# Optimization experiments

Measured on AMD Instinct MI355X. Metric: run time of the kernel, lower is better.

The kernel has to match this reference:

```python
import jax, jax.numpy as jnp
import numpy as np

SEQ, B, IN_DIM = 100, 2048, 64
MID_I, LATENT, V_MID, V_LAT, MID_O, OUT_DIM = 60, 20, 800, 50, 800, 512


def _lstm_cell(x, h, c, wih, whh, bih, bhh):
    # PyTorch gate order: i, f, g, o
    g = x @ wih.T + h @ whh.T + bih + bhh
    i, f, gg, o = jnp.split(g, 4, axis=-1)
    c = jax.nn.sigmoid(f) * c + jax.nn.sigmoid(i) * jnp.tanh(gg)
    h = jax.nn.sigmoid(o) * jnp.tanh(c)
    return h, c


def _lstm_seq(xs, wih, whh, bih, bhh, hid):
    b = xs.shape[1]
    init = (jnp.zeros((b, hid), xs.dtype), jnp.zeros((b, hid), xs.dtype))
    def step(carry, xt):
        h, c = _lstm_cell(xt, carry[0], carry[1], wih, whh, bih, bhh)
        return (h, c), h
    _, outs = jax.lax.scan(step, init, xs)
    return outs  # (seq, B, hid)


def setup_inputs() -> dict:
    key = jax.random.key(0)
    ks = iter(jax.random.split(key, 40))
    w = lambda shape: jax.random.normal(next(ks), shape, jnp.float32) * 0.05
    p = {}
    p['x'] = jax.random.normal(next(ks), (SEQ, B, IN_DIM), jnp.float32)
    p['fc1_wih'] = w((4 * MID_I, IN_DIM)); p['fc1_whh'] = w((4 * MID_I, MID_I))
    p['fc1_bih'] = w((4 * MID_I,)); p['fc1_bhh'] = w((4 * MID_I,))
    p['fc21_wih'] = w((4 * LATENT, MID_I)); p['fc21_whh'] = w((4 * LATENT, LATENT))
    p['fc21_bih'] = w((4 * LATENT,)); p['fc21_bhh'] = w((4 * LATENT,))
    p['lin1_w'] = w((V_MID, LATENT * SEQ)); p['lin1_b'] = w((V_MID,))
    p['lin2_w'] = w((V_LAT, V_MID)); p['lin2_b'] = w((V_LAT,))
    p['idlin_w'] = w((V_LAT, V_LAT)); p['idlin_b'] = w((V_LAT,))
    p['down1_w'] = w((LATENT, V_LAT)); p['down1_b'] = w((LATENT,))
    p['down2_w'] = w((LATENT, OUT_DIM)); p['down2_b'] = w((LATENT,))
    p['l3_wih'] = w((4 * V_LAT, LATENT)); p['l3_whh'] = w((4 * V_LAT, V_LAT))
    p['l3_bih'] = w((4 * V_LAT,)); p['l3_bhh'] = w((4 * V_LAT,))
    p['l4_wih'] = w((4 * MID_O, V_LAT)); p['l4_whh'] = w((4 * MID_O, MID_O))
    p['l4_bih'] = w((4 * MID_O,)); p['l4_bhh'] = w((4 * MID_O,))
    p['l5_wih'] = w((4 * OUT_DIM, MID_O)); p['l5_whh'] = w((4 * OUT_DIM, OUT_DIM))
    p['l5_bih'] = w((4 * OUT_DIM,)); p['l5_bhh'] = w((4 * OUT_DIM,))
    return p


def reference(x, fc1_wih, fc1_whh, fc1_bih, fc1_bhh,
              fc21_wih, fc21_whh, fc21_bih, fc21_bhh,
              lin1_w, lin1_b, lin2_w, lin2_b,
              idlin_w, idlin_b, down1_w, down1_b, down2_w, down2_b,
              l3_wih, l3_whh, l3_bih, l3_bhh,
              l4_wih, l4_whh, l4_bih, l4_bhh,
              l5_wih, l5_whh, l5_bih, l5_bhh):
    seq, b, _ = x.shape
    # encode
    h1 = jax.nn.relu(_lstm_seq(x, fc1_wih, fc1_whh, fc1_bih, fc1_bhh, MID_I))
    out21 = _lstm_seq(h1, fc21_wih, fc21_whh, fc21_bih, fc21_bhh, LATENT)
    flat = jnp.transpose(out21, (1, 2, 0)).reshape(b, -1)  # (B, latent*seq)
    mu = jax.nn.relu(flat @ lin1_w.T + lin1_b)
    mu = jax.nn.relu(mu @ lin2_w.T + lin2_b)  # (B, v_latent)
    # decode
    h_t = mu
    c_t = mu @ idlin_w.T + idlin_b
    out = mu @ down1_w.T + down1_b
    h2 = jnp.zeros((b, MID_O), mu.dtype); c2 = jnp.zeros((b, MID_O), mu.dtype)
    h3 = jnp.zeros((b, OUT_DIM), mu.dtype); c3 = jnp.zeros((b, OUT_DIM), mu.dtype)
    def step(carry, _):
        h_t, c_t, h2, c2, h3, c3, out = carry
        h_t, c_t = _lstm_cell(out, h_t, c_t, l3_wih, l3_whh, l3_bih, l3_bhh)
        h2, c2 = _lstm_cell(h_t, h2, c2, l4_wih, l4_whh, l4_bih, l4_bhh)
        h3, c3 = _lstm_cell(h2, h3, c3, l5_wih, l5_whh, l5_bih, l5_bhh)
        out = h3 @ down2_w.T + down2_b
        return (h_t, c_t, h2, c2, h3, c3, out), h3
    _, muTheta = jax.lax.scan(step, (h_t, c_t, h2, c2, h3, c3, out), None, length=seq)
    return muTheta, mu
```

## Files before the change

kernel.cpp:

```cpp
#include <hip/hip_runtime.h>
#include <cstdint>
#include <cstddef>

#define SEQ     100
#define BATCH   2048
#define IN_DIM  64
#define MID_I   60
#define LATENT  20
#define V_MID   800
#define V_LAT   50
#define MID_O   800
#define OUT_DIM 512

#define KP4  896
#define KP5  1344
#define KPL1 2048

using f32x4  = __attribute__((ext_vector_type(4))) float;
using u16x8  = __attribute__((ext_vector_type(8))) unsigned short;
using bf16x8 = __attribute__((ext_vector_type(8))) __bf16;
typedef _Float16 f16;
typedef _Float16 f16x8 __attribute__((ext_vector_type(8)));

__device__ __forceinline__ unsigned short f2bf(float x){
    unsigned u = __builtin_bit_cast(unsigned, x);
    u += 0x7FFFu + ((u >> 16) & 1u);
    return (unsigned short)(u >> 16);
}
__device__ __forceinline__ float bf2f(unsigned short b){
    unsigned u = ((unsigned)b) << 16; return __builtin_bit_cast(float, u);
}
__device__ __forceinline__ float sigm(float x){ return 1.f/(1.f+expf(-x)); }

typedef const __attribute__((address_space(1))) unsigned int* gas_ptr;
typedef __attribute__((address_space(3))) unsigned int* las_ptr;
__device__ __forceinline__ void gld16(const void* g, char* l) {
    __builtin_amdgcn_global_load_lds((gas_ptr)g, (las_ptr)l, 16, 0, 0);
}

constexpr int BM = 64, BN = 64, BK = 16;
template<bool RELU_A1, bool RELU_OUT>
__global__ __launch_bounds__(256)
void gemm2k(const float* __restrict__ A1, int K1,
            const float* __restrict__ A2, int K2,
            const float* __restrict__ W1, const float* __restrict__ W2,
            const float* __restrict__ b1, const float* __restrict__ b2,
            float* __restrict__ C, int M, int N)
{
    __shared__ float As[BK][BM + 1];
    __shared__ float Bs[BK][BN + 1];
    const int tx = threadIdx.x & 15;
    const int ty = threadIdx.x >> 4;
    const int n0 = blockIdx.x * BN;
    const int m0 = blockIdx.y * BM;

    float acc[4][4] = {};

    for (int src = 0; src < 2; ++src) {
        const float* A = src ? A2 : A1;
        const float* W = src ? W2 : W1;
        const int    K = src ? K2 : K1;
        if (A == nullptr || K == 0) continue;
        for (int k0 = 0; k0 < K; k0 += BK) {
            #pragma unroll
            for (int i = 0; i < 4; ++i) {
                int idx = threadIdx.x + i * 256;
                int k = idx & 15, m = idx >> 4;
                int gm = m0 + m, gk = k0 + k;
                float v = 0.f;
                if (gm < M && gk < K) v = A[(size_t)gm * K + gk];
                if (RELU_A1 && src == 0) v = fmaxf(v, 0.f);
                As[k][m] = v;
            }
            #pragma unroll
            for (int i = 0; i < 4; ++i) {
                int idx = threadIdx.x + i * 256;
                int k = idx & 15, n = idx >> 4;
                int gn = n0 + n, gk = k0 + k;
                float v = 0.f;
                if (gn < N && gk < K) v = W[(size_t)gn * K + gk];
                Bs[k][n] = v;
            }
            __syncthreads();
            #pragma unroll
            for (int kk = 0; kk < BK; ++kk) {
                float a[4], b[4];
                #pragma unroll
                for (int i = 0; i < 4; ++i) a[i] = As[kk][ty + i * 16];
                #pragma unroll
                for (int j = 0; j < 4; ++j) b[j] = Bs[kk][tx + j * 16];
                #pragma unroll
                for (int i = 0; i < 4; ++i)
                    #pragma unroll
                    for (int j = 0; j < 4; ++j)
                        acc[i][j] += a[i] * b[j];
            }
            __syncthreads();
        }
    }

    #pragma unroll
    for (int i = 0; i < 4; ++i) {
        int gm = m0 + ty + i * 16;
        if (gm >= M) continue;
        #pragma unroll
        for (int j = 0; j < 4; ++j) {
            int gn = n0 + tx + j * 16;
            if (gn >= N) continue;
            float v = acc[i][j];
            if (b1) v += b1[gn];
            if (b2) v += b2[gn];
            if (RELU_OUT) v = fmaxf(v, 0.f);
            C[(size_t)gm * N + gn] = v;
        }
    }
}

__global__ __launch_bounds__(256, 2)
void gemm_lin1(const unsigned short* __restrict__ Ah, const unsigned short* __restrict__ Al,
               const unsigned short* __restrict__ Bh, const unsigned short* __restrict__ Bl,
               int Kp, int Nstore, const float* __restrict__ bi, float* __restrict__ Cout)
{
    __shared__ __align__(16) char smem[32768];
    const int tid  = threadIdx.x;
    const int lane = tid & 63;
    const int wid  = tid >> 6;
    const int m0   = blockIdx.y * 128;
    const int n0   = blockIdx.x * 128;
    const int wr   = (wid >> 1) << 6;
    const int wc   = (wid & 1) << 6;
    const int fr   = lane & 15;
    const int fg   = lane >> 4;
    const int slotR = ((fg ^ (fr & 3)) << 4);

    const int r0 = 32 * wid + (lane >> 2);
    const int sl = (((lane & 3) ^ ((lane >> 2) & 3)) << 3);
    const unsigned short* gA0h = Ah + (size_t)(m0 + r0)      * Kp + sl;
    const unsigned short* gA1h = Ah + (size_t)(m0 + r0 + 16) * Kp + sl;
    const unsigned short* gA0l = Al + (size_t)(m0 + r0)      * Kp + sl;
    const unsigned short* gA1l = Al + (size_t)(m0 + r0 + 16) * Kp + sl;
    const unsigned short* gB0h = Bh + (size_t)(n0 + r0)      * Kp + sl;
    const unsigned short* gB1h = Bh + (size_t)(n0 + r0 + 16) * Kp + sl;
    const unsigned short* gB0l = Bl + (size_t)(n0 + r0)      * Kp + sl;
    const unsigned short* gB1l = Bl + (size_t)(n0 + r0 + 16) * Kp + sl;
    char* lA0h = smem +     0 + (2 * wid    ) * 1024;
    char* lA1h = smem +     0 + (2 * wid + 1) * 1024;
    char* lA0l = smem +  8192 + (2 * wid    ) * 1024;
    char* lA1l = smem +  8192 + (2 * wid + 1) * 1024;
    char* lB0h = smem + 16384 + (2 * wid    ) * 1024;
    char* lB1h = smem + 16384 + (2 * wid + 1) * 1024;
    char* lB0l = smem + 24576 + (2 * wid    ) * 1024;
    char* lB1l = smem + 24576 + (2 * wid + 1) * 1024;

    f32x4 acc[4][4];
    #pragma unroll
    for (int i = 0; i < 4; ++i)
        #pragma unroll
        for (int j = 0; j < 4; ++j) acc[i][j] = (f32x4){0.f, 0.f, 0.f, 0.f};

    for (int k0 = 0; k0 < Kp; k0 += 32) {
        __syncthreads();
        gld16(gA0h + k0, lA0h); gld16(gA1h + k0, lA1h);
        gld16(gA0l + k0, lA0l); gld16(gA1l + k0, lA1l);
        gld16(gB0h + k0, lB0h); gld16(gB1h + k0, lB1h);
        gld16(gB0l + k0, lB0l); gld16(gB1l + k0, lB1l);
        __syncthreads();

        bf16x8 ah[4], al[4];
        #pragma unroll
        for (int i = 0; i < 4; ++i) {
            int ro = (wr + i * 16 + fr) * 64 + slotR;
            ah[i] = *(const bf16x8*)(smem +        ro);
            al[i] = *(const bf16x8*)(smem + 8192 + ro);
        }
        #pragma unroll
        for (int j = 0; j < 4; ++j) {
            int ro = (wc + j * 16 + fr) * 64 + slotR;
            bf16x8 fbh = *(const bf16x8*)(smem + 16384 + ro);
            bf16x8 fbl = *(const bf16x8*)(smem + 24576 + ro);
            #pragma unroll
            for (int i = 0; i < 4; ++i) {
                acc[i][j] = __builtin_amdgcn_mfma_f32_16x16x32_bf16(ah[i], fbh, acc[i][j], 0, 0, 0);
                acc[i][j] = __builtin_amdgcn_mfma_f32_16x16x32_bf16(ah[i], fbl, acc[i][j], 0, 0, 0);
                acc[i][j] = __builtin_amdgcn_mfma_f32_16x16x32_bf16(al[i], fbh, acc[i][j], 0, 0, 0);
            }
        }
    }

    #pragma unroll
    for (int j = 0; j < 4; ++j) {
        int gc = n0 + wc + j * 16 + fr;
        if (gc >= Nstore) continue;
        float badd = bi[gc];
        #pragma unroll
        for (int i = 0; i < 4; ++i)
            #pragma unroll
            for (int r = 0; r < 4; ++r) {
                int gr = m0 + wr + i * 16 + fg * 4 + r;
                float v = fmaxf(acc[i][j][r] + badd, 0.f);
                Cout[(size_t)gr * Nstore + gc] = v;
            }
    }
}

template<int MODE>
__global__ __launch_bounds__(256, 3)
void gemm_dec(const f16* __restrict__ A, const f16* __restrict__ W,
              int Kp, int NK, int H, int NBX,
              const float* __restrict__ bp,
              float* __restrict__ cstate,
              f16* __restrict__ wr1, int st1, int off1,
              f16* __restrict__ wr2, int st2, int off2,
              float* __restrict__ out_t)
{
    __shared__ __align__(16) char smem[49152];
    const int qq      = NBX * 2;
    const int logical = (blockIdx.x & 7) * qq + (blockIdx.x >> 3);
    const int bx = logical >> 4;
    const int by = logical & 15;
    const int m0 = by * 128;
    const int n0 = bx * 128;

    const int tid  = threadIdx.x;
    const int lane = tid & 63;
    const int wid  = tid >> 6;
    const int wm   = wid >> 1;
    const int wn   = wid & 1;
    const int fr   = lane & 15;
    const int fg   = lane >> 4;
    const int swz  = (fg ^ (fr & 3) ^ ((fr >> 2) & 1)) * 16;

    const int rbase = 32 * wid;
    const int lrow  = lane >> 2;
    const int chnk  = (lane & 3) ^ ((lane >> 2) & 3) ^ ((lane >> 4) & 1);
    const f16* sA0 = A + (size_t)(m0 + rbase + lrow)      * Kp + chnk * 8;
    const f16* sA1 = A + (size_t)(m0 + rbase + 16 + lrow) * Kp + chnk * 8;
    const f16* sW0 = W + (size_t)(n0 + rbase + lrow)      * Kp + chnk * 8;
    const f16* sW1 = W + (size_t)(n0 + rbase + 16 + lrow) * Kp + chnk * 8;

    f32x4 acc[4][4];
    #pragma unroll
    for (int i = 0; i < 4; ++i)
        #pragma unroll
        for (int j = 0; j < 4; ++j) acc[i][j] = (f32x4){0.f, 0.f, 0.f, 0.f};

    auto stage = [&](int t, int buf) {
        const int kb = t * 32;
        char* bb = smem + buf * 16384;
        gld16(sA0 + kb, bb + rbase * 64);
        gld16(sA1 + kb, bb + (rbase + 16) * 64);
        gld16(sW0 + kb, bb + 8192 + rbase * 64);
        gld16(sW1 + kb, bb + 8192 + (rbase + 16) * 64);
    };

    stage(0, 0);
    stage(1, 1);

    int buf = 0;
    for (int t = 0; t < NK; ++t) {
        if (t + 1 < NK) asm volatile("s_waitcnt vmcnt(4)" ::: "memory");
        else            asm volatile("s_waitcnt vmcnt(0)" ::: "memory");
        __builtin_amdgcn_s_barrier();
        if (t + 2 < NK) stage(t + 2, (buf + 2) % 3);
        const char* bb = smem + buf * 16384;
        f16x8 af[4];
        #pragma unroll
        for (int i = 0; i < 4; ++i)
            af[i] = *(const f16x8*)(bb + (64 * wm + 16 * i + fr) * 64 + swz);
        #pragma unroll
        for (int j = 0; j < 4; ++j) {
            f16x8 vw = *(const f16x8*)(bb + 8192 + (64 * wn + 16 * j + fr) * 64 + swz);
            #pragma unroll
            for (int i = 0; i < 4; ++i)
                acc[i][j] = __builtin_amdgcn_mfma_f32_16x16x32_f16(af[i], vw, acc[i][j], 0, 0, 0);
        }
        buf = (buf + 1) % 3;
    }

    const int q4  = lane & 3;
    const bool qb0 = (lane & 1) != 0;
    const bool qb1 = (lane & 2) != 0;
    const int ubase = (n0 >> 2) + 16 * wn;
    const f32x4* bp4 = (const f32x4*)bp;

    #pragma unroll
    for (int i = 0; i < 4; ++i) {
        #pragma unroll
        for (int j = 0; j < 4; ++j) {
            float v0 = acc[i][j][0];
            float v1 = acc[i][j][1];
            float v2 = acc[i][j][2];
            float v3 = acc[i][j][3];
            {
                float s0 = qb0 ? v0 : v1;
                float s1 = qb0 ? v2 : v3;
                float r0 = __shfl_xor(s0, 1);
                float r1 = __shfl_xor(s1, 1);
                if (!qb0) { v1 = r0; v3 = r1; } else { v0 = r0; v2 = r1; }
            }
            {
                float s0 = qb1 ? v0 : v2;
                float s1 = qb1 ? v1 : v3;
                float r0 = __shfl_xor(s0, 2);
                float r1 = __shfl_xor(s1, 2);
                if (!qb1) { v2 = r0; v3 = r1; } else { v0 = r0; v1 = r1; }
            }
            const int unit = ubase + 4 * j + (fr >> 2);
            const int row  = m0 + 64 * wm + 16 * i + 4 * fg + q4;
            f32x4 bv = bp4[unit];
            float gi = v0 + bv[0], gf = v1 + bv[1], gg = v2 + bv[2], go = v3 + bv[3];
            size_t ci = (size_t)row * H + unit;
            float cn = sigm(gf) * cstate[ci] + sigm(gi) * tanhf(gg);
            float hn = sigm(go) * tanhf(cn);
            cstate[ci] = cn;
            f16 hh = (f16)hn;
            wr1[(size_t)row * st1 + off1 + unit] = hh;
            if (MODE == 1) wr2[(size_t)row * st2 + off2 + unit] = hh;
            if (MODE == 2) out_t[(size_t)row * H + unit] = hn;
        }
    }
}

__global__ void split_pack_lin1(const float* __restrict__ src,
                                unsigned short* __restrict__ dh, unsigned short* __restrict__ dl)
{
    int idx = blockIdx.x * blockDim.x + threadIdx.x;
    if (idx >= V_MID * LATENT * SEQ) return;
    int n = idx / (LATENT * SEQ), c = idx - n * (LATENT * SEQ);
    int l = c / SEQ, s = c - l * SEQ;
    float x = src[idx];
    unsigned short h = f2bf(x);
    size_t d = (size_t)n * KPL1 + s * LATENT + l;
    dh[d] = h;
    dl[d] = f2bf(x - bf2f(h));
}

__global__ void pack_f16(const float* __restrict__ src, int total, int K, int Kp,
                         int coff, int HU, f16* __restrict__ dh)
{
    int idx = blockIdx.x * blockDim.x + threadIdx.x;
    if (idx >= total) return;
    int n = idx / K, k = idx - n * K;
    int p = (n % HU) * 4 + n / HU;
    dh[(size_t)p * Kp + coff + k] = (f16)src[idx];
}

__global__ void bias_pack(const float* __restrict__ bih, const float* __restrict__ bhh,
                          int H, float* __restrict__ bp)
{
    int idx = blockIdx.x * blockDim.x + threadIdx.x;
    if (idx >= 4 * H) return;
    int g = idx / H, u = idx - g * H;
    bp[u * 4 + g] = bih[idx] + bhh[idx];
}

__global__ __launch_bounds__(256)
void enc_rec1(const float* __restrict__ xp, int T,
              const float* __restrict__ whh,
              float* __restrict__ hbuf, float* __restrict__ cbuf,
              float* __restrict__ h1relu)
{
    __shared__ float Wt[60][240];
    __shared__ float hs[4][60];
    for (int idx = threadIdx.x; idx < 240 * 60; idx += 256) {
        int n = idx / 60, k = idx % 60;
        Wt[k][n] = whh[idx];
    }
    int wid = threadIdx.x >> 6, lane = threadIdx.x & 63;
    int b = blockIdx.x * 4 + wid;
    float h = 0.f, c = 0.f;
    if (lane < 60) {
        h = hbuf[(size_t)b * 60 + lane];
        c = cbuf[(size_t)b * 60 + lane];
        hs[wid][lane] = h;
    }
    __syncthreads();
    for (int t = 0; t < T; ++t) {
        if (lane < 60) {
            const float* xr = xp + ((size_t)t * BATCH + b) * 240;
            float gi = xr[lane], gf = xr[60 + lane], gg = xr[120 + lane], go = xr[180 + lane];
            for (int k = 0; k < 60; ++k) {
                float v = hs[wid][k];
                gi += v * Wt[k][lane];
                gf += v * Wt[k][60 + lane];
                gg += v * Wt[k][120 + lane];
                go += v * Wt[k][180 + lane];
            }
            float cn = sigm(gf) * c + sigm(gi) * tanhf(gg);
            float hn = sigm(go) * tanhf(cn);
            c = cn; h = hn;
            h1relu[((size_t)t * BATCH + b) * 60 + lane] = fmaxf(hn, 0.f);
        }
        __syncthreads();
        if (lane < 60) hs[wid][lane] = h;
        __syncthreads();
    }
    if (lane < 60) {
        hbuf[(size_t)b * 60 + lane] = h;
        cbuf[(size_t)b * 60 + lane] = c;
    }
}

__global__ __launch_bounds__(256)
void enc_rec21(const float* __restrict__ xp, int T, int t0,
               const float* __restrict__ whh,
               float* __restrict__ hbuf, float* __restrict__ cbuf,
               unsigned short* __restrict__ fh, unsigned short* __restrict__ fl)
{
    __shared__ float Wt[20][80];
    __shared__ float hs[4][20];
    for (int idx = threadIdx.x; idx < 80 * 20; idx += 256) {
        int n = idx / 20, k = idx % 20;
        Wt[k][n] = whh[idx];
    }
    int wid = threadIdx.x >> 6, lane = threadIdx.x & 63;
    int b = blockIdx.x * 4 + wid;
    float h = 0.f, c = 0.f;
    if (lane < 20) {
        h = hbuf[(size_t)b * 20 + lane];
        c = cbuf[(size_t)b * 20 + lane];
        hs[wid][lane] = h;
    }
    __syncthreads();
    for (int t = 0; t < T; ++t) {
        if (lane < 20) {
            const float* xr = xp + ((size_t)t * BATCH + b) * 80;
            float gi = xr[lane], gf = xr[20 + lane], gg = xr[40 + lane], go = xr[60 + lane];
            for (int k = 0; k < 20; ++k) {
                float v = hs[wid][k];
                gi += v * Wt[k][lane];
                gf += v * Wt[k][20 + lane];
                gg += v * Wt[k][40 + lane];
                go += v * Wt[k][60 + lane];
            }
            float cn = sigm(gf) * c + sigm(gi) * tanhf(gg);
            float hn = sigm(go) * tanhf(cn);
            c = cn; h = hn;
            int col = (t0 + t) * 20 + lane;
            unsigned short hh = f2bf(hn);
            fh[(size_t)b * KPL1 + col] = hh;
            fl[(size_t)b * KPL1 + col] = f2bf(hn - bf2f(hh));
        }
        __syncthreads();
        if (lane < 20) hs[wid][lane] = h;
        __syncthreads();
    }
    if (lane < 20) {
        hbuf[(size_t)b * 20 + lane] = h;
        cbuf[(size_t)b * 20 + lane] = c;
    }
}

__global__ __launch_bounds__(256)
void dec_l3(const float* __restrict__ outb,
            const float* __restrict__ wih,
            const float* __restrict__ whh,
            const float* __restrict__ bih, const float* __restrict__ bhh,
            float* __restrict__ h_t, float* __restrict__ c_t,
            f16* __restrict__ a4)
{
    __shared__ float Wt[70][200];
    __shared__ float xin[4][70];
    for (int idx = threadIdx.x; idx < 200 * 20; idx += 256) {
        int n = idx / 20, k = idx % 20;
        Wt[k][n] = wih[idx];
    }
    for (int idx = threadIdx.x; idx < 200 * 50; idx += 256) {
        int n = idx / 50, k = idx % 50;
        Wt[20 + k][n] = whh[idx];
    }
    int wid = threadIdx.x >> 6, lane = threadIdx.x & 63;
    int b = blockIdx.x * 4 + wid;
    if (lane < 20) xin[wid][lane]      = outb[(size_t)b * 20 + lane];
    if (lane < 50) xin[wid][20 + lane] = h_t[(size_t)b * 50 + lane];
    __syncthreads();
    if (lane < 50) {
        float gi = bih[lane] + bhh[lane];
        float gf = bih[50 + lane] + bhh[50 + lane];
        float gg = bih[100 + lane] + bhh[100 + lane];
        float go = bih[150 + lane] + bhh[150 + lane];
        for (int k = 0; k < 70; ++k) {
            float v = xin[wid][k];
            gi += v * Wt[k][lane];
            gf += v * Wt[k][50 + lane];
            gg += v * Wt[k][100 + lane];
            go += v * Wt[k][150 + lane];
        }
        float cold = c_t[(size_t)b * 50 + lane];
        float cn = sigm(gf) * cold + sigm(gi) * tanhf(gg);
        float hn = sigm(go) * tanhf(cn);
        c_t[(size_t)b * 50 + lane] = cn;
        h_t[(size_t)b * 50 + lane] = hn;
        a4[(size_t)b * KP4 + lane] = (f16)hn;
    }
}

__global__ __launch_bounds__(1024)
void dec_step3(const float* __restrict__ h3prev,
               const float* __restrict__ w2, const float* __restrict__ b2,
               const float* __restrict__ wih, const float* __restrict__ whh,
               const float* __restrict__ bih, const float* __restrict__ bhh,
               float* __restrict__ h_t, float* __restrict__ c_t,
               f16* __restrict__ a4)
{
    __shared__ float w2s[20][512];
    __shared__ float W3[70][200];
    __shared__ float xb[16][80];
    const int tid  = threadIdx.x;
    const int lane = tid & 63;
    const int w    = tid >> 6;
    const int row  = blockIdx.x * 16 + w;

    for (int idx = tid; idx < 20 * 512; idx += 1024)
        w2s[idx >> 9][idx & 511] = w2[idx];
    for (int idx = tid; idx < 200 * 20; idx += 1024) {
        int n = idx / 20, k = idx - n * 20;
        W3[k][n] = wih[idx];
    }
    for (int idx = tid; idx < 200 * 50; idx += 1024) {
        int n = idx / 50, k = idx - n * 50;
        W3[20 + k][n] = whh[idx];
    }
    if (lane < 50) xb[w][20 + lane] = h_t[(size_t)row * 50 + lane];

    float hreg[8];
    const float* hrow = h3prev + (size_t)row * 512;
    #pragma unroll
    for (int c = 0; c < 8; ++c) hreg[c] = hrow[lane + 64 * c];
    __syncthreads();

    #pragma unroll 4
    for (int n = 0; n < 20; ++n) {
        float s = 0.f;
        #pragma unroll
        for (int c = 0; c < 8; ++c) s += hreg[c] * w2s[n][lane + 64 * c];
        #pragma unroll
        for (int o = 32; o; o >>= 1) s += __shfl_xor(s, o);
        if (lane == 0) xb[w][n] = s + b2[n];
    }
    __syncthreads();

    if (lane < 50) {
        const int u = lane;
        float gi = bih[u] + bhh[u];
        float gf = bih[50 + u] + bhh[50 + u];
        float gg = bih[100 + u] + bhh[100 + u];
        float go = bih[150 + u] + bhh[150 + u];
        for (int k = 0; k < 70; ++k) {
            float v = xb[w][k];
            gi += v * W3[k][u];
            gf += v * W3[k][50 + u];
            gg += v * W3[k][100 + u];
            go += v * W3[k][150 + u];
        }
        size_t ci = (size_t)row * 50 + u;
        float cn = sigm(gf) * c_t[ci] + sigm(gi) * tanhf(gg);
        float hn = sigm(go) * tanhf(cn);
        c_t[ci] = cn;
        h_t[ci] = hn;
        a4[(size_t)row * KP4 + u] = (f16)hn;
    }
}

extern "C" void kernel_launch(void* const* d_in, const int* in_sizes, int n_in,
                              void* d_out_v, int out_size, void* d_ws, size_t ws_size,
                              hipStream_t stream)
{
    const float* x        = (const float*)d_in[0];
    const float* fc1_wih  = (const float*)d_in[1];
    const float* fc1_whh  = (const float*)d_in[2];
    const float* fc1_bih  = (const float*)d_in[3];
    const float* fc1_bhh  = (const float*)d_in[4];
    const float* fc21_wih = (const float*)d_in[5];
    const float* fc21_whh = (const float*)d_in[6];
    const float* fc21_bih = (const float*)d_in[7];
    const float* fc21_bhh = (const float*)d_in[8];
    const float* lin1_w   = (const float*)d_in[9];
    const float* lin1_b   = (const float*)d_in[10];
    const float* lin2_w   = (const float*)d_in[11];
    const float* lin2_b   = (const float*)d_in[12];
    const float* idlin_w  = (const float*)d_in[13];
    const float* idlin_b  = (const float*)d_in[14];
    const float* down1_w  = (const float*)d_in[15];
    const float* down1_b  = (const float*)d_in[16];
    const float* down2_w  = (const float*)d_in[17];
    const float* down2_b  = (const float*)d_in[18];
    const float* l3_wih   = (const float*)d_in[19];
    const float* l3_whh   = (const float*)d_in[20];
    const float* l3_bih   = (const float*)d_in[21];
    const float* l3_bhh   = (const float*)d_in[22];
    const float* l4_wih   = (const float*)d_in[23];
    const float* l4_whh   = (const float*)d_in[24];
    const float* l4_bih   = (const float*)d_in[25];
    const float* l4_bhh   = (const float*)d_in[26];
    const float* l5_wih   = (const float*)d_in[27];
    const float* l5_whh   = (const float*)d_in[28];
    const float* l5_bih   = (const float*)d_in[29];
    const float* l5_bhh   = (const float*)d_in[30];
    float* out = (float*)d_out_v;

    char* base = (char*)d_ws;
    size_t off = 0;
    auto alloc = [&](size_t bytes) -> void* {
        off = (off + 255) & ~(size_t)255;
        void* p = base + off;
        off += bytes;
        return p;
    };

    size_t us_begin = (off + 255) & ~(size_t)255;
    f16* W4h = (f16*)alloc((size_t)3200 * KP4 * 2);
    f16* W5h = (f16*)alloc((size_t)2048 * KP5 * 2);
    unsigned short* L1h = (unsigned short*)alloc((size_t)896 * KPL1 * 2);
    unsigned short* L1l = (unsigned short*)alloc((size_t)896 * KPL1 * 2);
    unsigned short* Fh  = (unsigned short*)alloc((size_t)BATCH * KPL1 * 2);
    unsigned short* Fl  = (unsigned short*)alloc((size_t)BATCH * KPL1 * 2);
    f16* A4[2]; f16* A5[2];
    for (int p = 0; p < 2; ++p) {
        A4[p] = (f16*)alloc((size_t)BATCH * KP4 * 2);
        A5[p] = (f16*)alloc((size_t)BATCH * KP5 * 2);
    }
    size_t us_end = off;

    size_t fz_begin = (off + 255) & ~(size_t)255;
    float* c2   = (float*)alloc((size_t)BATCH * MID_O * 4);
    float* c3   = (float*)alloc((size_t)BATCH * OUT_DIM * 4);
    float* hb1  = (float*)alloc((size_t)BATCH * MID_I * 4);
    float* cb1  = (float*)alloc((size_t)BATCH * MID_I * 4);
    float* hb21 = (float*)alloc((size_t)BATCH * LATENT * 4);
    float* cb21 = (float*)alloc((size_t)BATCH * LATENT * 4);
    size_t fz_end = off;

    float* bp4   = (float*)alloc((size_t)4 * MID_O * 4);
    float* bp5   = (float*)alloc((size_t)4 * OUT_DIM * 4);
    float* mu1   = (float*)alloc((size_t)BATCH * V_MID * 4);
    float* mu    = (float*)alloc((size_t)BATCH * V_LAT * 4);
    float* h_t   = (float*)alloc((size_t)BATCH * V_LAT * 4);
    float* c_t   = (float*)alloc((size_t)BATCH * V_LAT * 4);
    float* outb  = (float*)alloc((size_t)BATCH * LATENT * 4);
    const int CH = 20;
    float* xp1c  = (float*)alloc((size_t)CH * BATCH * 4 * MID_I * 4);
    float* h1rc  = (float*)alloc((size_t)CH * BATCH * MID_I * 4);
    float* xp21c = (float*)alloc((size_t)CH * BATCH * 4 * LATENT * 4);

    hipMemsetAsync(base + us_begin, 0, us_end - us_begin, stream);
    hipMemsetAsync(base + fz_begin, 0, fz_end - fz_begin, stream);

    pack_f16<<<(3200 * 50  + 255) / 256, 256, 0, stream>>>(l4_wih, 3200 * 50,  50,  KP4, 0,   800, W4h);
    pack_f16<<<(3200 * 800 + 255) / 256, 256, 0, stream>>>(l4_whh, 3200 * 800, 800, KP4, 64,  800, W4h);
    pack_f16<<<(2048 * 800 + 255) / 256, 256, 0, stream>>>(l5_wih, 2048 * 800, 800, KP5, 0,   512, W5h);
    pack_f16<<<(2048 * 512 + 255) / 256, 256, 0, stream>>>(l5_whh, 2048 * 512, 512, KP5, 832, 512, W5h);
    split_pack_lin1<<<(V_MID * LATENT * SEQ + 255) / 256, 256, 0, stream>>>(lin1_w, L1h, L1l);
    bias_pack<<<(4 * MID_O   + 255) / 256, 256, 0, stream>>>(l4_bih, l4_bhh, MID_O,   bp4);
    bias_pack<<<(4 * OUT_DIM + 255) / 256, 256, 0, stream>>>(l5_bih, l5_bhh, OUT_DIM, bp5);

    for (int c0 = 0; c0 < SEQ; c0 += CH) {
        {
            dim3 g((4 * MID_I + BN - 1) / BN, CH * BATCH / BM);
            gemm2k<false, false><<<g, 256, 0, stream>>>(
                x + (size_t)c0 * BATCH * IN_DIM, IN_DIM, nullptr, 0,
                fc1_wih, nullptr, fc1_bih, fc1_bhh, xp1c, CH * BATCH, 4 * MID_I);
        }
        enc_rec1<<<BATCH / 4, 256, 0, stream>>>(xp1c, CH, fc1_whh, hb1, cb1, h1rc);
        {
            dim3 g((4 * LATENT + BN - 1) / BN, CH * BATCH / BM);
            gemm2k<false, false><<<g, 256, 0, stream>>>(
                h1rc, MID_I, nullptr, 0,
                fc21_wih, nullptr, fc21_bih, fc21_bhh, xp21c, CH * BATCH, 4 * LATENT);
        }
        enc_rec21<<<BATCH / 4, 256, 0, stream>>>(xp21c, CH, c0, fc21_whh, hb21, cb21, Fh, Fl);
    }

    {
        dim3 g(7, 16);
        gemm_lin1<<<g, 256, 0, stream>>>(Fh, Fl, L1h, L1l, KPL1, V_MID, lin1_b, mu1);
    }
    {
        dim3 g((V_LAT + BN - 1) / BN, BATCH / BM);
        gemm2k<false, true><<<g, 256, 0, stream>>>(mu1, V_MID, nullptr, 0,
            lin2_w, nullptr, lin2_b, nullptr, mu, BATCH, V_LAT);
    }

    hipMemcpyAsync(h_t, mu, (size_t)BATCH * V_LAT * 4, hipMemcpyDeviceToDevice, stream);
    {
        dim3 g(1, BATCH / BM);
        gemm2k<false, false><<<g, 256, 0, stream>>>(mu, V_LAT, nullptr, 0,
            idlin_w, nullptr, idlin_b, nullptr, c_t, BATCH, V_LAT);
        gemm2k<false, false><<<g, 256, 0, stream>>>(mu, V_LAT, nullptr, 0,
            down1_w, nullptr, down1_b, nullptr, outb, BATCH, LATENT);
    }

    for (int t = 0; t < SEQ; ++t) {
        const int p = t & 1;
        if (t == 0) {
            dec_l3<<<BATCH / 4, 256, 0, stream>>>(outb, l3_wih, l3_whh, l3_bih, l3_bhh,
                                                  h_t, c_t, A4[0]);
        } else {
            dec_step3<<<BATCH / 16, 1024, 0, stream>>>(
                out + (size_t)(t - 1) * BATCH * OUT_DIM,
                down2_w, down2_b, l3_wih, l3_whh, l3_bih, l3_bhh,
                h_t, c_t, A4[p]);
        }
        {
            gemm_dec<1><<<dim3(400), 256, 0, stream>>>(
                A4[p], W4h, KP4, KP4 / 32, MID_O, 25, bp4, c2,
                A4[p ^ 1], KP4, 64,
                A5[p], KP5, 0,
                nullptr);
        }
        {
            gemm_dec<2><<<dim3(256), 256, 0, stream>>>(
                A5[p], W5h, KP5, KP5 / 32, OUT_DIM, 16, bp5, c3,
                A5[p ^ 1], KP5, 832,
                nullptr, 0, 0,
                out + (size_t)t * BATCH * OUT_DIM);
        }
    }

    hipMemcpyAsync(out + (size_t)SEQ * BATCH * OUT_DIM, mu,
                   (size_t)BATCH * V_LAT * 4, hipMemcpyDeviceToDevice, stream);
}
```

Baseline: 8.884 ms.

## Stage gemm_dec epilogue through LDS, use fast exp/tanh, halve dec_step3 blocks

The gemm_dec epilogue no longer shuffles gate values across lanes. It writes the accumulator tiles to shared memory in two halves and reads them back so each thread owns one unit column, which makes the cstate and h stores coalesced. Sigmoid and tanh now use __expf-based formulas in every LSTM kernel, trading some accuracy for cheaper transcendentals. dec_step3 drops from 1024 to 512 threads per block with twice as many blocks, which repeats the shared-weight staging more often but may improve scheduling.

```diff
diff --git a/kernel.cpp b/kernel.cpp
--- a/kernel.cpp
+++ b/kernel.cpp
@@ -30,7 +30,8 @@
 __device__ __forceinline__ float bf2f(unsigned short b){
     unsigned u = ((unsigned)b) << 16; return __builtin_bit_cast(float, u);
 }
-__device__ __forceinline__ float sigm(float x){ return 1.f/(1.f+expf(-x)); }
+__device__ __forceinline__ float sigm(float x){ return 1.f/(1.f+__expf(-x)); }
+__device__ __forceinline__ float tanh_f(float x){ return 1.f - 2.f/(__expf(2.f*x)+1.f); }
 
 typedef const __attribute__((address_space(1))) unsigned int* gas_ptr;
 typedef __attribute__((address_space(3))) unsigned int* las_ptr;
@@ -277,41 +278,36 @@
         buf = (buf + 1) % 3;
     }
 
-    const int q4  = lane & 3;
-    const bool qb0 = (lane & 1) != 0;
-    const bool qb1 = (lane & 2) != 0;
-    const int ubase = (n0 >> 2) + 16 * wn;
+    float* gt = (float*)smem;
+    const int u32 = tid & 31;
+    const int r8  = tid >> 5;
+    const int unit = (n0 >> 2) + u32;
     const f32x4* bp4 = (const f32x4*)bp;
+    const f32x4 bv = bp4[unit];
 
     #pragma unroll
-    for (int i = 0; i < 4; ++i) {
-        #pragma unroll
-        for (int j = 0; j < 4; ++j) {
-            float v0 = acc[i][j][0];
-            float v1 = acc[i][j][1];
-            float v2 = acc[i][j][2];
-            float v3 = acc[i][j][3];
-            {
-                float s0 = qb0 ? v0 : v1;
-                float s1 = qb0 ? v2 : v3;
-                float r0 = __shfl_xor(s0, 1);
-                float r1 = __shfl_xor(s1, 1);
-                if (!qb0) { v1 = r0; v3 = r1; } else { v0 = r0; v2 = r1; }
-            }
-            {
-                float s0 = qb1 ? v0 : v2;
-                float s1 = qb1 ? v1 : v3;
-                float r0 = __shfl_xor(s0, 2);
-                float r1 = __shfl_xor(s1, 2);
-                if (!qb1) { v2 = r0; v3 = r1; } else { v0 = r0; v1 = r1; }
-            }
-            const int unit = ubase + 4 * j + (fr >> 2);
-            const int row  = m0 + 64 * wm + 16 * i + 4 * fg + q4;
-            f32x4 bv = bp4[unit];
-            float gi = v0 + bv[0], gf = v1 + bv[1], gg = v2 + bv[2], go = v3 + bv[3];
+    for (int half = 0; half < 2; ++half) {
+        __syncthreads();
+        if (wm == half) {
+            #pragma unroll
+            for (int i = 0; i < 4; ++i)
+                #pragma unroll
+                for (int j = 0; j < 4; ++j)
+                    #pragma unroll
+                    for (int r = 0; r < 4; ++r)
+                        gt[(16*i + 4*fg + r) * 132 + 64*wn + 16*j + fr] = acc[i][j][r];
+        }
+        __syncthreads();
+        #pragma unroll
+        for (int kk = 0; kk < 8; ++kk) {
+            const int lr  = 8 * kk + r8;
+            const int row = m0 + 64 * half + lr;
+            f32x4 g = *(const f32x4*)(gt + lr * 132 + u32 * 4);
+            float gi = g[0] + bv[0], gf = g[1] + bv[1];
+            float gg = g[2] + bv[2], go = g[3] + bv[3];
             size_t ci = (size_t)row * H + unit;
-            float cn = sigm(gf) * cstate[ci] + sigm(gi) * tanhf(gg);
-            float hn = sigm(go) * tanhf(cn);
+            float cn = sigm(gf) * cstate[ci] + sigm(gi) * tanh_f(gg);
+            float hn = sigm(go) * tanh_f(cn);
             cstate[ci] = cn;
             f16 hh = (f16)hn;
             wr1[(size_t)row * st1 + off1 + unit] = hh;
@@ -386,8 +382,8 @@
                 gg += v * Wt[k][120 + lane];
                 go += v * Wt[k][180 + lane];
             }
-            float cn = sigm(gf) * c + sigm(gi) * tanhf(gg);
-            float hn = sigm(go) * tanhf(cn);
+            float cn = sigm(gf) * c + sigm(gi) * tanh_f(gg);
+            float hn = sigm(go) * tanh_f(cn);
             c = cn; h = hn;
             h1relu[((size_t)t * BATCH + b) * 60 + lane] = fmaxf(hn, 0.f);
         }
@@ -433,8 +429,8 @@
                 gg += v * Wt[k][40 + lane];
                 go += v * Wt[k][60 + lane];
             }
-            float cn = sigm(gf) * c + sigm(gi) * tanhf(gg);
-            float hn = sigm(go) * tanhf(cn);
+            float cn = sigm(gf) * c + sigm(gi) * tanh_f(gg);
+            float hn = sigm(go) * tanh_f(cn);
             c = cn; h = hn;
             int col = (t0 + t) * 20 + lane;
             unsigned short hh = f2bf(hn);
@@ -487,15 +483,15 @@
             go += v * Wt[k][150 + lane];
         }
         float cold = c_t[(size_t)b * 50 + lane];
-        float cn = sigm(gf) * cold + sigm(gi) * tanhf(gg);
-        float hn = sigm(go) * tanhf(cn);
+        float cn = sigm(gf) * cold + sigm(gi) * tanh_f(gg);
+        float hn = sigm(go) * tanh_f(cn);
         c_t[(size_t)b * 50 + lane] = cn;
         h_t[(size_t)b * 50 + lane] = hn;
         a4[(size_t)b * KP4 + lane] = (f16)hn;
     }
 }
 
-__global__ __launch_bounds__(1024)
+__global__ __launch_bounds__(512)
 void dec_step3(const float* __restrict__ h3prev,
                const float* __restrict__ w2, const float* __restrict__ b2,
                const float* __restrict__ wih, const float* __restrict__ whh,
@@ -505,19 +501,19 @@
 {
     __shared__ float w2s[20][512];
     __shared__ float W3[70][200];
-    __shared__ float xb[16][80];
+    __shared__ float xb[8][80];
     const int tid  = threadIdx.x;
     const int lane = tid & 63;
     const int w    = tid >> 6;
-    const int row  = blockIdx.x * 16 + w;
-
-    for (int idx = tid; idx < 20 * 512; idx += 1024)
+    const int row  = blockIdx.x * 8 + w;
+
+    for (int idx = tid; idx < 20 * 512; idx += 512)
         w2s[idx >> 9][idx & 511] = w2[idx];
-    for (int idx = tid; idx < 200 * 20; idx += 1024) {
+    for (int idx = tid; idx < 200 * 20; idx += 512) {
         int n = idx / 20, k = idx - n * 20;
         W3[k][n] = wih[idx];
     }
-    for (int idx = tid; idx < 200 * 50; idx += 1024) {
+    for (int idx = tid; idx < 200 * 50; idx += 512) {
         int n = idx / 50, k = idx - n * 50;
         W3[20 + k][n] = whh[idx];
     }
@@ -554,8 +550,8 @@
             go += v * W3[k][150 + u];
         }
         size_t ci = (size_t)row * 50 + u;
-        float cn = sigm(gf) * c_t[ci] + sigm(gi) * tanhf(gg);
-        float hn = sigm(go) * tanhf(cn);
+        float cn = sigm(gf) * c_t[ci] + sigm(gi) * tanh_f(gg);
+        float hn = sigm(go) * tanh_f(cn);
         c_t[ci] = cn;
         h_t[ci] = hn;
         a4[(size_t)row * KP4 + u] = (f16)hn;
@@ -696,7 +692,7 @@
             dec_l3<<<BATCH / 4, 256, 0, stream>>>(outb, l3_wih, l3_whh, l3_bih, l3_bhh,
                                                   h_t, c_t, A4[0]);
         } else {
-            dec_step3<<<BATCH / 16, 1024, 0, stream>>>(
+            dec_step3<<<BATCH / 8, 512, 0, stream>>>(
                 out + (size_t)(t - 1) * BATCH * OUT_DIM,
                 down2_w, down2_b, l3_wih, l3_whh, l3_bih, l3_bhh,
                 h_t, c_t, A4[p]);
```

Measured after the change: 7.671 ms. 13.6% less time.
